# Optimization experiments

Hardware: AMD Instinct MI355X
Metric: run time of the kernel (lower is better)

The kernel has to match this reference:

```python
import jax, jax.numpy as jnp
import numpy as np

E = 8
TOP_K = 2
CAP_FACTOR = 1.25
MIN_CAP = 4
SCORE_SCALE = 1.0


def _ffn(x, w1, b1, w2, b2):
    # torch ExpertFFN: w2(gelu(w1(x))), exact (erf) gelu
    return jax.nn.gelu(x @ w1 + b1, approximate=False) @ w2 + b2


def setup_inputs() -> dict:
    key = jax.random.key(0)
    ks = jax.random.split(key, 6)
    B, S, D, I = 4, 2048, 1024, 4096
    std = 0.02
    return {
        'x': jax.random.normal(ks[0], (B, S, D), jnp.float32),
        'Wr': jax.random.normal(ks[1], (E, D), jnp.float32) * std,
        'W1': jax.random.normal(ks[2], (E, D, I), jnp.float32) * std,
        'b1': jnp.zeros((E, I), jnp.float32),
        'W2': jax.random.normal(ks[3], (E, I, D), jnp.float32) * std,
        'b2': jnp.zeros((E, D), jnp.float32),
        'fw1': jax.random.normal(ks[4], (D, I), jnp.float32) * std,
        'fb1': jnp.zeros((I,), jnp.float32),
        'fw2': jax.random.normal(ks[5], (I, D), jnp.float32) * std,
        'fb2': jnp.zeros((D,), jnp.float32),
    }


def reference(x, Wr, W1, b1, W2, b2, fw1, fb1, fw2, fb2):
    B, S, D = x.shape
    T = B * S
    x_flat = x.reshape(T, D)

    # ---- router ----
    logits = (x_flat @ Wr.T) * SCORE_SCALE            # [T, E]
    probs = jax.nn.softmax(logits, axis=-1)
    topk_scores, topk_experts = jax.lax.top_k(probs, TOP_K)   # [T,k]
    topk_scores = topk_scores / jnp.clip(
        topk_scores.sum(-1, keepdims=True), 1e-9, None)

    cap = max(int(CAP_FACTOR * (T * TOP_K / E)), MIN_CAP)

    # fallback output for all tokens (used only at overflow positions)
    y_fb = _ffn(x_flat, fw1, fb1, fw2, fb2)           # [T, D]

    y_flat = jnp.zeros_like(x_flat)
    fallback = jnp.zeros((T,), bool)  # route_threshold = 0 -> starts all False
    tok_ids = jnp.arange(T, dtype=jnp.int32)

    # sequential per-expert dispatch (matches torch loop semantics exactly,
    # including overwrite-on-overflow ordering)
    for e in range(E):
        match = topk_experts == e                     # [T, k]
        elig = match.any(-1) & ~fallback              # [T]
        pos = jnp.cumsum(elig) - 1                    # position among eligible, token order
        kept = elig & (pos < cap)
        overflow = elig & (pos >= cap)

        # capacity-limited gather: fixed-size [cap] buffer of token indices
        slot = jnp.where(kept, pos, cap)              # invalids dumped in slot `cap`
        buf = jnp.zeros((cap + 1,), jnp.int32).at[slot].set(tok_ids)
        vmask = jnp.zeros((cap + 1,), bool).at[slot].set(kept)
        idx = buf[:cap]                               # [cap]
        valid = vmask[:cap]                           # [cap]

        x_e = x_flat[idx]                             # [cap, D]
        y_e = _ffn(x_e, W1[e], b1[e], W2[e], b2[e])   # [cap, D]
        w_tok = (topk_scores * match).sum(-1)         # [T] (top-k experts distinct)
        w = jnp.where(valid, w_tok[idx], 0.0)         # [cap]
        y_flat = y_flat.at[idx].add(y_e * w[:, None])

        # overflow tokens: overwrite with dense fallback, mark as done
        y_flat = jnp.where(overflow[:, None], y_fb, y_flat)
        fallback = fallback | overflow

    return y_flat.reshape(B, S, D)
```

## Files before the change

kernel.cpp:

```cpp
#include <hip/hip_runtime.h>
#include <hip/hip_bf16.h>
#include <cstdint>
#include <cstddef>

#define TT 8192
#define DD 1024
#define II 4096
#define EE 8
#define CAP 2560

#define BM 128
#define BN 128
#define BK 32
#define LDK 40

typedef __attribute__((ext_vector_type(4))) float f32x4_t;
typedef __attribute__((ext_vector_type(8))) short bf16x8_t;

static __device__ __forceinline__ unsigned short f2bf(float f) {
    __hip_bfloat16 h = __float2bfloat16(f);
    return *reinterpret_cast<unsigned short*>(&h);
}
static __device__ __forceinline__ float geluf(float v) {
    return 0.5f * v * (1.0f + erff(v * 0.70710678118654752f));
}

__global__ __launch_bounds__(256) void transpose_cvt(
    const float* __restrict__ in, unsigned short* __restrict__ out, int R, int C) {
    __shared__ float tile[32][33];
    size_t mb = (size_t)blockIdx.z * (size_t)R * (size_t)C;
    in += mb; out += mb;
    int cb = blockIdx.x * 32, rb = blockIdx.y * 32;
    int tx = threadIdx.x, ty = threadIdx.y;
#pragma unroll
    for (int j = 0; j < 4; ++j)
        tile[ty + j * 8][tx] = in[(size_t)(rb + ty + j * 8) * C + cb + tx];
    __syncthreads();
#pragma unroll
    for (int j = 0; j < 4; ++j)
        out[(size_t)(cb + ty + j * 8) * R + rb + tx] = f2bf(tile[tx][ty + j * 8]);
}

__global__ __launch_bounds__(256) void router_kernel(
    const float* __restrict__ x, const float* __restrict__ Wr,
    int* __restrict__ e0a, int* __restrict__ e1a,
    float* __restrict__ w0a, float* __restrict__ w1a) {
    int t = blockIdx.x * 4 + (threadIdx.x >> 6);
    int lane = threadIdx.x & 63;
    const float* xr = x + (size_t)t * DD;
    float acc[EE];
#pragma unroll
    for (int e = 0; e < EE; ++e) acc[e] = 0.f;
    for (int c = 0; c < DD; c += 64) {
        float xv = xr[c + lane];
#pragma unroll
        for (int e = 0; e < EE; ++e) acc[e] += xv * Wr[e * DD + c + lane];
    }
#pragma unroll
    for (int e = 0; e < EE; ++e) {
        float v = acc[e];
#pragma unroll
        for (int off = 32; off > 0; off >>= 1) v += __shfl_xor(v, off, 64);
        acc[e] = v;
    }
    if (lane == 0) {
        int b0 = 0; float m0 = acc[0];
#pragma unroll
        for (int e = 1; e < EE; ++e) if (acc[e] > m0) { m0 = acc[e]; b0 = e; }
        int b1 = -1; float m1 = -3.4e38f;
#pragma unroll
        for (int e = 0; e < EE; ++e) if (e != b0 && acc[e] > m1) { m1 = acc[e]; b1 = e; }
        float w0 = 1.f / (1.f + expf(m1 - m0));
        e0a[t] = b0; e1a[t] = b1; w0a[t] = w0; w1a[t] = 1.f - w0;
    }
}

__global__ __launch_bounds__(1024) void assign_kernel(
    const int* __restrict__ e0a, const int* __restrict__ e1a,
    const float* __restrict__ w0a, const float* __restrict__ w1a,
    int* __restrict__ idxb, float* __restrict__ wslb,
    int* __restrict__ fbidx, int* __restrict__ counts) {
    __shared__ int sc[1024];
    __shared__ int ns[EE];
    const int t = threadIdx.x;
    int e0v[8], e1v[8]; float w0v[8], w1v[8];
    bool fbv[8]; int sA[8], sB[8];
#pragma unroll
    for (int j = 0; j < 8; ++j) {
        int tok = t * 8 + j;
        e0v[j] = e0a[tok]; e1v[j] = e1a[tok];
        w0v[j] = w0a[tok]; w1v[j] = w1a[tok];
        fbv[j] = false; sA[j] = -1; sB[j] = -1;
    }
    for (int e = 0; e < EE; ++e) {
        int lp[8]; int c = 0; bool el[8];
#pragma unroll
        for (int j = 0; j < 8; ++j) {
            el[j] = (!fbv[j]) && (e0v[j] == e || e1v[j] == e);
            lp[j] = c; c += el[j] ? 1 : 0;
        }
        sc[t] = c; __syncthreads();
        for (int off = 1; off < 1024; off <<= 1) {
            int add = (t >= off) ? sc[t - off] : 0;
            __syncthreads();
            sc[t] += add;
            __syncthreads();
        }
        int base = sc[t] - c;
        int total = sc[1023];
#pragma unroll
        for (int j = 0; j < 8; ++j) {
            if (el[j]) {
                int pos = base + lp[j];
                if (pos < CAP) {
                    int s = e * CAP + pos;
                    idxb[s] = t * 8 + j;
                    wslb[s] = (e0v[j] == e) ? w0v[j] : w1v[j];
                    if (sA[j] < 0) sA[j] = s; else sB[j] = s;
                } else {
                    fbv[j] = true;
                }
            }
        }
        if (t == 0) ns[e] = total < CAP ? total : CAP;
        __syncthreads();
    }
    for (int s = t; s < EE * CAP; s += 1024) {
        int e = s / CAP, pos = s - e * CAP;
        if (pos >= ns[e]) { idxb[s] = 0; wslb[s] = 0.f; }
    }
#pragma unroll
    for (int j = 0; j < 8; ++j) {
        if (fbv[j]) {
            if (sA[j] >= 0) wslb[sA[j]] = 0.f;
            if (sB[j] >= 0) wslb[sB[j]] = 0.f;
        }
    }
    int lp[8]; int c = 0;
#pragma unroll
    for (int j = 0; j < 8; ++j) { lp[j] = c; c += fbv[j] ? 1 : 0; }
    sc[t] = c; __syncthreads();
    for (int off = 1; off < 1024; off <<= 1) {
        int add = (t >= off) ? sc[t - off] : 0;
        __syncthreads();
        sc[t] += add;
        __syncthreads();
    }
    int base = sc[t] - c;
    int total = sc[1023];
#pragma unroll
    for (int j = 0; j < 8; ++j)
        if (fbv[j]) fbidx[base + lp[j]] = t * 8 + j;
    for (int s = t; s < TT; s += 1024)
        if (s >= total) fbidx[s] = 0;
    if (t == 0) {
        for (int e = 0; e < EE; ++e) counts[e] = ns[e];
        counts[EE] = total;
    }
}

template <int MODE>
__global__ __launch_bounds__(256) void gemm_kernel(
    const float* __restrict__ xsrc,
    const unsigned short* __restrict__ Asrc,
    const unsigned short* __restrict__ Bt,
    const float* __restrict__ bias,
    unsigned short* __restrict__ Hout,
    float* __restrict__ dout,
    const int* __restrict__ idxp,
    const float* __restrict__ wslp,
    const int* __restrict__ counts,
    int e_base, int chunk_base) {
    constexpr bool IS_G1 = (MODE == 0 || MODE == 2);
    constexpr bool IS_EXPERT = (MODE == 0 || MODE == 1);
    constexpr int K = IS_G1 ? DD : II;

    const int z = blockIdx.z;
    const int e = e_base + z;
    const int m_base = blockIdx.x * BM;
    const int n_base = blockIdx.y * BN;

    const int cnt = IS_EXPERT ? counts[e] : counts[EE];
    if (IS_EXPERT) { if (m_base >= cnt) return; }
    else           { if (chunk_base + m_base >= cnt) return; }

    __shared__ alignas(16) unsigned short As[BM * LDK];
    __shared__ alignas(16) unsigned short Bs[BN * LDK];

    const int tid = threadIdx.x;
    const int lane = tid & 63;
    const int wv = tid >> 6;
    const int wm = (wv & 1) * 64;
    const int wn = (wv >> 1) * 64;
    const int l15 = lane & 15;
    const int quad = lane >> 4;

    const unsigned short* BtE;
    if (MODE == 0)      BtE = Bt + (size_t)e * II * DD;
    else if (MODE == 1) BtE = Bt + (size_t)e * DD * II;
    else                BtE = Bt;

    const int ar  = tid >> 3;
    const int ac  = (tid & 7) * 4;
    const int ar2 = tid >> 2;
    const int ac2 = (tid & 3) * 8;

    const float* aptr[4];
    const unsigned short* aptr2[2];
    if (IS_G1) {
#pragma unroll
        for (int p = 0; p < 4; ++p) {
            int slot = m_base + p * 32 + ar;
            int tok = (MODE == 0) ? idxp[e * CAP + slot] : idxp[chunk_base + slot];
            aptr[p] = xsrc + (size_t)tok * DD + ac;
        }
    } else {
        const unsigned short* Ab = (MODE == 1) ? (Asrc + (size_t)z * CAP * II) : Asrc;
#pragma unroll
        for (int p = 0; p < 2; ++p)
            aptr2[p] = Ab + (size_t)(m_base + p * 64 + ar2) * II + ac2;
    }

    f32x4_t acc[4][4];
#pragma unroll
    for (int i = 0; i < 4; ++i)
#pragma unroll
        for (int j = 0; j < 4; ++j) acc[i][j] = (f32x4_t){0.f, 0.f, 0.f, 0.f};

    for (int k0 = 0; k0 < K; k0 += BK) {
        if (IS_G1) {
#pragma unroll
            for (int p = 0; p < 4; ++p) {
                int row = p * 32 + ar;
                float4 v = *(const float4*)(aptr[p] + k0);
                unsigned long long pk =
                      (unsigned long long)f2bf(v.x)
                    | ((unsigned long long)f2bf(v.y) << 16)
                    | ((unsigned long long)f2bf(v.z) << 32)
                    | ((unsigned long long)f2bf(v.w) << 48);
                *(unsigned long long*)&As[row * LDK + ac] = pk;
            }
        } else {
#pragma unroll
            for (int p = 0; p < 2; ++p) {
                int row = p * 64 + ar2;
                uint4 v = *(const uint4*)(aptr2[p] + k0);
                *(uint4*)&As[row * LDK + ac2] = v;
            }
        }
#pragma unroll
        for (int p = 0; p < 2; ++p) {
            int n = p * 64 + ar2;
            uint4 v = *(const uint4*)(BtE + (size_t)(n_base + n) * K + k0 + ac2);
            *(uint4*)&Bs[n * LDK + ac2] = v;
        }
        __syncthreads();
        {
            const int koff = quad * 8;
            bf16x8_t af[4], bfv[4];
#pragma unroll
            for (int i = 0; i < 4; ++i)
                af[i] = *(const bf16x8_t*)&As[(wm + i * 16 + l15) * LDK + koff];
#pragma unroll
            for (int j = 0; j < 4; ++j)
                bfv[j] = *(const bf16x8_t*)&Bs[(wn + j * 16 + l15) * LDK + koff];
#pragma unroll
            for (int i = 0; i < 4; ++i)
#pragma unroll
                for (int j = 0; j < 4; ++j)
                    acc[i][j] = __builtin_amdgcn_mfma_f32_16x16x32_bf16(
                        af[i], bfv[j], acc[i][j], 0, 0, 0);
        }
        __syncthreads();
    }

#pragma unroll
    for (int i = 0; i < 4; ++i) {
        const int mrow0 = wm + i * 16 + quad * 4;
#pragma unroll
        for (int j = 0; j < 4; ++j) {
            const int ncol = n_base + wn + j * 16 + l15;
            float bv;
            if (MODE == 0)      bv = bias[(size_t)e * II + ncol];
            else if (MODE == 1) bv = bias[(size_t)e * DD + ncol];
            else                bv = bias[ncol];
#pragma unroll
            for (int r = 0; r < 4; ++r) {
                const int slot = m_base + mrow0 + r;
                float v = acc[i][j][r] + bv;
                if (MODE == 0) {
                    Hout[(size_t)(z * CAP + slot) * II + ncol] = f2bf(geluf(v));
                } else if (MODE == 2) {
                    Hout[(size_t)slot * II + ncol] = f2bf(geluf(v));
                } else if (MODE == 1) {
                    float w = wslp[e * CAP + slot];
                    if (w != 0.f) {
                        int tok = idxp[e * CAP + slot];
                        atomicAdd(&dout[(size_t)tok * DD + ncol], v * w);
                    }
                } else {
                    int rg = chunk_base + slot;
                    if (rg < cnt) {
                        int tok = idxp[rg];
                        dout[(size_t)tok * DD + ncol] = v;
                    }
                }
            }
        }
    }
}

extern "C" void kernel_launch(void* const* d_in, const int* in_sizes, int n_in,
                              void* d_out, int out_size, void* d_ws, size_t ws_size,
                              hipStream_t stream) {
    const float* x   = (const float*)d_in[0];
    const float* Wr  = (const float*)d_in[1];
    const float* W1  = (const float*)d_in[2];
    const float* b1  = (const float*)d_in[3];
    const float* W2  = (const float*)d_in[4];
    const float* b2  = (const float*)d_in[5];
    const float* fw1 = (const float*)d_in[6];
    const float* fb1 = (const float*)d_in[7];
    const float* fw2 = (const float*)d_in[8];
    const float* fb2 = (const float*)d_in[9];
    float* out = (float*)d_out;

    char* ws = (char*)d_ws;
    size_t off = 0;
    auto alloc = [&](size_t bytes) -> void* {
        void* p = ws + off;
        off += (bytes + 255) & ~(size_t)255;
        return p;
    };
    unsigned short* W1t  = (unsigned short*)alloc((size_t)EE * DD * II * 2);
    unsigned short* W2t  = (unsigned short*)alloc((size_t)EE * II * DD * 2);
    unsigned short* fw1t = (unsigned short*)alloc((size_t)DD * II * 2);
    unsigned short* fw2t = (unsigned short*)alloc((size_t)II * DD * 2);
    int*   e0a   = (int*)alloc(TT * 4);
    int*   e1a   = (int*)alloc(TT * 4);
    float* w0a   = (float*)alloc(TT * 4);
    float* w1a   = (float*)alloc(TT * 4);
    int*   idxb  = (int*)alloc(EE * CAP * 4);
    float* wslb  = (float*)alloc(EE * CAP * 4);
    int*   fbidx = (int*)alloc(TT * 4);
    int*   counts = (int*)alloc(64);

    size_t perExpert = (size_t)CAP * II * 2;
    size_t remain = (ws_size > off) ? (ws_size - off) : 0;
    int G = (int)(remain / perExpert);
    if (G < 1) G = 1;
    if (G > EE) G = EE;
    unsigned short* H = (unsigned short*)(ws + off);

    hipMemsetAsync(d_out, 0, (size_t)TT * DD * sizeof(float), stream);

    transpose_cvt<<<dim3(II / 32, DD / 32, EE), dim3(32, 8), 0, stream>>>(W1, W1t, DD, II);
    transpose_cvt<<<dim3(DD / 32, II / 32, EE), dim3(32, 8), 0, stream>>>(W2, W2t, II, DD);
    transpose_cvt<<<dim3(II / 32, DD / 32, 1),  dim3(32, 8), 0, stream>>>(fw1, fw1t, DD, II);
    transpose_cvt<<<dim3(DD / 32, II / 32, 1),  dim3(32, 8), 0, stream>>>(fw2, fw2t, II, DD);

    router_kernel<<<TT / 4, 256, 0, stream>>>(x, Wr, e0a, e1a, w0a, w1a);
    assign_kernel<<<1, 1024, 0, stream>>>(e0a, e1a, w0a, w1a, idxb, wslb, fbidx, counts);

    for (int eb = 0; eb < EE; eb += G) {
        int g = (EE - eb < G) ? (EE - eb) : G;
        gemm_kernel<0><<<dim3(CAP / BM, II / BN, g), 256, 0, stream>>>(
            x, nullptr, W1t, b1, H, nullptr, idxb, wslb, counts, eb, 0);
        gemm_kernel<1><<<dim3(CAP / BM, DD / BN, g), 256, 0, stream>>>(
            nullptr, H, W2t, b2, nullptr, out, idxb, wslb, counts, eb, 0);
    }
    for (int c = 0; c < 4; ++c) {
        gemm_kernel<2><<<dim3(CAP / BM, II / BN, 1), 256, 0, stream>>>(
            x, nullptr, fw1t, fb1, H, nullptr, fbidx, nullptr, counts, 0, c * CAP);
        gemm_kernel<3><<<dim3(CAP / BM, DD / BN, 1), 256, 0, stream>>>(
            nullptr, H, fw2t, fb2, nullptr, out, fbidx, nullptr, counts, 0, c * CAP);
    }
    (void)in_sizes; (void)n_in; (void)out_size;
}
```

Before: 1.076 ms.

## Use direct global-to-LDS loads with swizzle, pre-convert x to bf16, batch fallback GEMMs

The GEMM main loop now uses global_load_lds to copy bf16 tiles straight into an unpadded LDS layout with an XOR swizzle, replacing the register-staged copy and padding. x is converted to bf16 once up front so the first GEMM gathers bf16 rows instead of converting fp32 on every tile. The assign kernel's block scan is replaced with wave shuffle scans, and the four fallback chunks run as one launch using the z dimension when enough workspace exists. Risks are LDS bank conflicts or alignment problems if the swizzle doesn't match the layout written by the direct loads, and there is still no double buffering.

After: 955.6 us. -11.2%, faster.

```diff
diff --git a/kernel.cpp b/kernel.cpp
--- a/kernel.cpp
+++ b/kernel.cpp
@@ -12,7 +12,6 @@
 #define BM 128
 #define BN 128
 #define BK 32
-#define LDK 40
 
 typedef __attribute__((ext_vector_type(4))) float f32x4_t;
 typedef __attribute__((ext_vector_type(8))) short bf16x8_t;
@@ -23,6 +22,23 @@
 }
 static __device__ __forceinline__ float geluf(float v) {
     return 0.5f * v * (1.0f + erff(v * 0.70710678118654752f));
+}
+
+static __device__ __forceinline__ void gl_lds16(const void* g, void* l) {
+    __builtin_amdgcn_global_load_lds(
+        (__attribute__((address_space(1))) unsigned int*)g,
+        (__attribute__((address_space(3))) unsigned int*)l, 16, 0, 0);
+}
+
+__global__ __launch_bounds__(256) void cvt_x(
+    const float* __restrict__ in, unsigned short* __restrict__ out) {
+    int i = (blockIdx.x * 256 + threadIdx.x) * 8;
+    float4 a = *(const float4*)(in + i);
+    float4 b = *(const float4*)(in + i + 4);
+    union { unsigned short s[8]; uint4 u; } pk;
+    pk.s[0] = f2bf(a.x); pk.s[1] = f2bf(a.y); pk.s[2] = f2bf(a.z); pk.s[3] = f2bf(a.w);
+    pk.s[4] = f2bf(b.x); pk.s[5] = f2bf(b.y); pk.s[6] = f2bf(b.z); pk.s[7] = f2bf(b.w);
+    *(uint4*)(out + i) = pk.u;
 }
 
 __global__ __launch_bounds__(256) void transpose_cvt(
@@ -80,9 +96,11 @@
     const float* __restrict__ w0a, const float* __restrict__ w1a,
     int* __restrict__ idxb, float* __restrict__ wslb,
     int* __restrict__ fbidx, int* __restrict__ counts) {
-    __shared__ int sc[1024];
+    __shared__ int wsum[16];
     __shared__ int ns[EE];
     const int t = threadIdx.x;
+    const int lane = t & 63;
+    const int wv = t >> 6;
     int e0v[8], e1v[8]; float w0v[8], w1v[8];
     bool fbv[8]; int sA[8], sB[8];
 #pragma unroll
@@ -99,15 +117,22 @@
             el[j] = (!fbv[j]) && (e0v[j] == e || e1v[j] == e);
             lp[j] = c; c += el[j] ? 1 : 0;
         }
-        sc[t] = c; __syncthreads();
-        for (int off = 1; off < 1024; off <<= 1) {
-            int add = (t >= off) ? sc[t - off] : 0;
-            __syncthreads();
-            sc[t] += add;
-            __syncthreads();
-        }
-        int base = sc[t] - c;
-        int total = sc[1023];
+        int incl = c;
+#pragma unroll
+        for (int off = 1; off < 64; off <<= 1) {
+            int v = __shfl_up(incl, off, 64);
+            if (lane >= off) incl += v;
+        }
+        if (lane == 63) wsum[wv] = incl;
+        __syncthreads();
+        int wbase = 0, total = 0;
+#pragma unroll
+        for (int u = 0; u < 16; ++u) {
+            int v = wsum[u];
+            total += v;
+            if (u < wv) wbase += v;
+        }
+        int base = wbase + incl - c;
 #pragma unroll
         for (int j = 0; j < 8; ++j) {
             if (el[j]) {
@@ -139,19 +164,26 @@
     int lp[8]; int c = 0;
 #pragma unroll
     for (int j = 0; j < 8; ++j) { lp[j] = c; c += fbv[j] ? 1 : 0; }
-    sc[t] = c; __syncthreads();
-    for (int off = 1; off < 1024; off <<= 1) {
-        int add = (t >= off) ? sc[t - off] : 0;
-        __syncthreads();
-        sc[t] += add;
-        __syncthreads();
-    }
-    int base = sc[t] - c;
-    int total = sc[1023];
+    int incl = c;
+#pragma unroll
+    for (int off = 1; off < 64; off <<= 1) {
+        int v = __shfl_up(incl, off, 64);
+        if (lane >= off) incl += v;
+    }
+    if (lane == 63) wsum[wv] = incl;
+    __syncthreads();
+    int wbase = 0, total = 0;
+#pragma unroll
+    for (int u = 0; u < 16; ++u) {
+        int v = wsum[u];
+        total += v;
+        if (u < wv) wbase += v;
+    }
+    int base = wbase + incl - c;
 #pragma unroll
     for (int j = 0; j < 8; ++j)
         if (fbv[j]) fbidx[base + lp[j]] = t * 8 + j;
-    for (int s = t; s < TT; s += 1024)
+    for (int s = t; s < 4 * CAP; s += 1024)
         if (s >= total) fbidx[s] = 0;
     if (t == 0) {
         for (int e = 0; e < EE; ++e) counts[e] = ns[e];
@@ -161,8 +193,7 @@
 
 template <int MODE>
 __global__ __launch_bounds__(256) void gemm_kernel(
-    const float* __restrict__ xsrc,
-    const unsigned short* __restrict__ Asrc,
+    const unsigned short* __restrict__ Abase,
     const unsigned short* __restrict__ Bt,
     const float* __restrict__ bias,
     unsigned short* __restrict__ Hout,
@@ -177,15 +208,16 @@
 
     const int z = blockIdx.z;
     const int e = e_base + z;
+    const int ch0 = chunk_base + z * CAP;
     const int m_base = blockIdx.x * BM;
     const int n_base = blockIdx.y * BN;
 
     const int cnt = IS_EXPERT ? counts[e] : counts[EE];
     if (IS_EXPERT) { if (m_base >= cnt) return; }
-    else           { if (chunk_base + m_base >= cnt) return; }
-
-    __shared__ alignas(16) unsigned short As[BM * LDK];
-    __shared__ alignas(16) unsigned short Bs[BN * LDK];
+    else           { if (ch0 + m_base >= cnt) return; }
+
+    __shared__ alignas(16) unsigned short As[BM * BK];
+    __shared__ alignas(16) unsigned short Bs[BN * BK];
 
     const int tid = threadIdx.x;
     const int lane = tid & 63;
@@ -200,25 +232,27 @@
     else if (MODE == 1) BtE = Bt + (size_t)e * DD * II;
     else                BtE = Bt;
 
-    const int ar  = tid >> 3;
-    const int ac  = (tid & 7) * 4;
-    const int ar2 = tid >> 2;
-    const int ac2 = (tid & 3) * 8;
-
-    const float* aptr[4];
-    const unsigned short* aptr2[2];
-    if (IS_G1) {
-#pragma unroll
-        for (int p = 0; p < 4; ++p) {
-            int slot = m_base + p * 32 + ar;
-            int tok = (MODE == 0) ? idxp[e * CAP + slot] : idxp[chunk_base + slot];
-            aptr[p] = xsrc + (size_t)tok * DD + ac;
-        }
-    } else {
-        const unsigned short* Ab = (MODE == 1) ? (Asrc + (size_t)z * CAP * II) : Asrc;
-#pragma unroll
-        for (int p = 0; p < 2; ++p)
-            aptr2[p] = Ab + (size_t)(m_base + p * 64 + ar2) * II + ac2;
+    const int lrow = lane >> 2;
+    const int kc = (lane & 3) ^ ((lrow >> 2) & 3);
+    const unsigned short* aP[2];
+    const unsigned short* bP[2];
+#pragma unroll
+    for (int p = 0; p < 2; ++p) {
+        int r = wv * 32 + p * 16 + lrow;
+        int slot = m_base + r;
+        int arow;
+        if (MODE == 0)      arow = idxp[e * CAP + slot];
+        else if (MODE == 2) arow = idxp[ch0 + slot];
+        else                arow = z * CAP + slot;
+        aP[p] = Abase + (size_t)arow * K + kc * 8;
+        int nrow = n_base + r;
+        bP[p] = BtE + (size_t)nrow * K + kc * 8;
+    }
+    unsigned short* lA[2]; unsigned short* lB[2];
+#pragma unroll
+    for (int p = 0; p < 2; ++p) {
+        lA[p] = &As[(wv * 32 + p * 16) * BK];
+        lB[p] = &Bs[(wv * 32 + p * 16) * BK];
     }
 
     f32x4_t acc[4][4];
@@ -227,50 +261,25 @@
 #pragma unroll
         for (int j = 0; j < 4; ++j) acc[i][j] = (f32x4_t){0.f, 0.f, 0.f, 0.f};
 
+    const int sw = (l15 >> 2) & 3;
     for (int k0 = 0; k0 < K; k0 += BK) {
-        if (IS_G1) {
-#pragma unroll
-            for (int p = 0; p < 4; ++p) {
-                int row = p * 32 + ar;
-                float4 v = *(const float4*)(aptr[p] + k0);
-                unsigned long long pk =
-                      (unsigned long long)f2bf(v.x)
-                    | ((unsigned long long)f2bf(v.y) << 16)
-                    | ((unsigned long long)f2bf(v.z) << 32)
-                    | ((unsigned long long)f2bf(v.w) << 48);
-                *(unsigned long long*)&As[row * LDK + ac] = pk;
-            }
-        } else {
-#pragma unroll
-            for (int p = 0; p < 2; ++p) {
-                int row = p * 64 + ar2;
-                uint4 v = *(const uint4*)(aptr2[p] + k0);
-                *(uint4*)&As[row * LDK + ac2] = v;
-            }
-        }
-#pragma unroll
-        for (int p = 0; p < 2; ++p) {
-            int n = p * 64 + ar2;
-            uint4 v = *(const uint4*)(BtE + (size_t)(n_base + n) * K + k0 + ac2);
-            *(uint4*)&Bs[n * LDK + ac2] = v;
-        }
+        gl_lds16(aP[0], lA[0]); gl_lds16(aP[1], lA[1]);
+        gl_lds16(bP[0], lB[0]); gl_lds16(bP[1], lB[1]);
+        aP[0] += BK; aP[1] += BK; bP[0] += BK; bP[1] += BK;
         __syncthreads();
-        {
-            const int koff = quad * 8;
-            bf16x8_t af[4], bfv[4];
-#pragma unroll
-            for (int i = 0; i < 4; ++i)
-                af[i] = *(const bf16x8_t*)&As[(wm + i * 16 + l15) * LDK + koff];
+        bf16x8_t af[4], bfv[4];
+#pragma unroll
+        for (int i = 0; i < 4; ++i)
+            af[i] = *(const bf16x8_t*)&As[(wm + i * 16 + l15) * BK + ((quad ^ sw) * 8)];
+#pragma unroll
+        for (int j = 0; j < 4; ++j)
+            bfv[j] = *(const bf16x8_t*)&Bs[(wn + j * 16 + l15) * BK + ((quad ^ sw) * 8)];
+#pragma unroll
+        for (int i = 0; i < 4; ++i)
 #pragma unroll
             for (int j = 0; j < 4; ++j)
-                bfv[j] = *(const bf16x8_t*)&Bs[(wn + j * 16 + l15) * LDK + koff];
-#pragma unroll
-            for (int i = 0; i < 4; ++i)
-#pragma unroll
-                for (int j = 0; j < 4; ++j)
-                    acc[i][j] = __builtin_amdgcn_mfma_f32_16x16x32_bf16(
-                        af[i], bfv[j], acc[i][j], 0, 0, 0);
-        }
+                acc[i][j] = __builtin_amdgcn_mfma_f32_16x16x32_bf16(
+                    af[i], bfv[j], acc[i][j], 0, 0, 0);
         __syncthreads();
     }
 
@@ -288,10 +297,8 @@
             for (int r = 0; r < 4; ++r) {
                 const int slot = m_base + mrow0 + r;
                 float v = acc[i][j][r] + bv;
-                if (MODE == 0) {
+                if (MODE == 0 || MODE == 2) {
                     Hout[(size_t)(z * CAP + slot) * II + ncol] = f2bf(geluf(v));
-                } else if (MODE == 2) {
-                    Hout[(size_t)slot * II + ncol] = f2bf(geluf(v));
                 } else if (MODE == 1) {
                     float w = wslp[e * CAP + slot];
                     if (w != 0.f) {
@@ -299,7 +306,7 @@
                         atomicAdd(&dout[(size_t)tok * DD + ncol], v * w);
                     }
                 } else {
-                    int rg = chunk_base + slot;
+                    int rg = ch0 + slot;
                     if (rg < cnt) {
                         int tok = idxp[rg];
                         dout[(size_t)tok * DD + ncol] = v;
@@ -336,13 +343,14 @@
     unsigned short* W2t  = (unsigned short*)alloc((size_t)EE * II * DD * 2);
     unsigned short* fw1t = (unsigned short*)alloc((size_t)DD * II * 2);
     unsigned short* fw2t = (unsigned short*)alloc((size_t)II * DD * 2);
+    unsigned short* xbf  = (unsigned short*)alloc((size_t)TT * DD * 2);
     int*   e0a   = (int*)alloc(TT * 4);
     int*   e1a   = (int*)alloc(TT * 4);
     float* w0a   = (float*)alloc(TT * 4);
     float* w1a   = (float*)alloc(TT * 4);
     int*   idxb  = (int*)alloc(EE * CAP * 4);
     float* wslb  = (float*)alloc(EE * CAP * 4);
-    int*   fbidx = (int*)alloc(TT * 4);
+    int*   fbidx = (int*)alloc(4 * CAP * 4);
     int*   counts = (int*)alloc(64);
 
     size_t perExpert = (size_t)CAP * II * 2;
@@ -354,6 +362,7 @@
 
     hipMemsetAsync(d_out, 0, (size_t)TT * DD * sizeof(float), stream);
 
+    cvt_x<<<TT * DD / (256 * 8), 256, 0, stream>>>(x, xbf);
     transpose_cvt<<<dim3(II / 32, DD / 32, EE), dim3(32, 8), 0, stream>>>(W1, W1t, DD, II);
     transpose_cvt<<<dim3(DD / 32, II / 32, EE), dim3(32, 8), 0, stream>>>(W2, W2t, II, DD);
     transpose_cvt<<<dim3(II / 32, DD / 32, 1),  dim3(32, 8), 0, stream>>>(fw1, fw1t, DD, II);
@@ -365,15 +374,22 @@
     for (int eb = 0; eb < EE; eb += G) {
         int g = (EE - eb < G) ? (EE - eb) : G;
         gemm_kernel<0><<<dim3(CAP / BM, II / BN, g), 256, 0, stream>>>(
-            x, nullptr, W1t, b1, H, nullptr, idxb, wslb, counts, eb, 0);
+            xbf, W1t, b1, H, nullptr, idxb, wslb, counts, eb, 0);
         gemm_kernel<1><<<dim3(CAP / BM, DD / BN, g), 256, 0, stream>>>(
-            nullptr, H, W2t, b2, nullptr, out, idxb, wslb, counts, eb, 0);
-    }
-    for (int c = 0; c < 4; ++c) {
-        gemm_kernel<2><<<dim3(CAP / BM, II / BN, 1), 256, 0, stream>>>(
-            x, nullptr, fw1t, fb1, H, nullptr, fbidx, nullptr, counts, 0, c * CAP);
-        gemm_kernel<3><<<dim3(CAP / BM, DD / BN, 1), 256, 0, stream>>>(
-            nullptr, H, fw2t, fb2, nullptr, out, fbidx, nullptr, counts, 0, c * CAP);
+            H, W2t, b2, nullptr, out, idxb, wslb, counts, eb, 0);
+    }
+    if (G >= 4) {
+        gemm_kernel<2><<<dim3(CAP / BM, II / BN, 4), 256, 0, stream>>>(
+            xbf, fw1t, fb1, H, nullptr, fbidx, nullptr, counts, 0, 0);
+        gemm_kernel<3><<<dim3(CAP / BM, DD / BN, 4), 256, 0, stream>>>(
+            H, fw2t, fb2, nullptr, out, fbidx, nullptr, counts, 0, 0);
+    } else {
+        for (int c = 0; c < 4; ++c) {
+            gemm_kernel<2><<<dim3(CAP / BM, II / BN, 1), 256, 0, stream>>>(
+                xbf, fw1t, fb1, H, nullptr, fbidx, nullptr, counts, 0, c * CAP);
+            gemm_kernel<3><<<dim3(CAP / BM, DD / BN, 1), 256, 0, stream>>>(
+                H, fw2t, fb2, nullptr, out, fbidx, nullptr, counts, 0, c * CAP);
+        }
     }
     (void)in_sizes; (void)n_in; (void)out_size;
 }
```
